# Performance work log

Hardware: AMD Instinct MI355X
Metric: run time of the kernel (lower is better)

## Reference

```python
import jax, jax.numpy as jnp
import numpy as np

B, D, H, E, K = 8192, 1024, 256, 16, 4


def setup_inputs() -> dict:
    key = jax.random.key(0)
    ks = jax.random.split(key, 6)
    s_d = D ** -0.5
    s_h = H ** -0.5
    return {
        "x": jax.random.normal(ks[0], (B, D), dtype=jnp.float32),
        "route_w": jax.random.normal(ks[1], (E, D), dtype=jnp.float32) * s_d,
        "w1": jax.random.normal(ks[2], (E, H, D), dtype=jnp.float32) * s_d,
        "b1": jax.random.normal(ks[3], (E, H), dtype=jnp.float32) * s_d,
        "w2": jax.random.normal(ks[4], (E, D, H), dtype=jnp.float32) * s_h,
        "b2": jax.random.normal(ks[5], (E, D), dtype=jnp.float32) * s_h,
    }


def _moe_forward(x, route_w, w1, b1, w2, b2):
    # Router: logits (B, E) -> top-k softmax weights scattered back to (B, E).
    logits = x @ route_w.T
    top_vals, top_idx = jax.lax.top_k(logits, K)
    top_w = jax.nn.softmax(top_vals, axis=-1)
    rows = jnp.arange(x.shape[0])[:, None]
    weights = jnp.zeros_like(logits).at[rows, top_idx].set(top_w)  # (B, E)

    # Experts: out = sum_e w[:, e] * relu(relu(x W1e^T + b1e) W2e^T + b2e)
    # Non-selected experts have weight 0, so dense-then-weight matches the
    # original masked gather/scatter math exactly (dropout = 0).
    def step(out, params_e):
        W1, bb1, W2, bb2, we = params_e
        h = jax.nn.relu(x @ W1.T + bb1)       # (B, H)
        y = jax.nn.relu(h @ W2.T + bb2)       # (B, D)
        return out + y * we[:, None], None

    out0 = jnp.zeros_like(x)
    out, _ = jax.lax.scan(step, out0, (w1, b1, w2, b2, weights.T))
    return out


def reference(x, route_w, w1, b1, w2, b2):
    return _moe_forward(x, route_w, w1, b1, w2, b2)
```

## Files before the change

### kernel.cpp

```cpp
#include <hip/hip_runtime.h>
#include <stdint.h>

typedef unsigned short u16;
typedef __attribute__((ext_vector_type(8))) short bf16x8;
typedef __attribute__((ext_vector_type(4))) float f32x4;
typedef __attribute__((ext_vector_type(8))) u16 u16x8;
typedef __attribute__((ext_vector_type(4))) u16 u16x4;

#define NTOK 8192
#define DDIM 1024
#define HDIM 256
#define NEXP 16
#define MAXT 272
#define MAXSLOT (MAXT * 128)

__device__ __forceinline__ u16 f2bf(float f) {
  uint32_t u = __builtin_bit_cast(uint32_t, f);
  u += 0x7FFFu + ((u >> 16) & 1u);
  return (u16)(u >> 16);
}
__device__ __forceinline__ float bf2f(u16 h) {
  return __builtin_bit_cast(float, (uint32_t)h << 16);
}

__device__ __forceinline__ void gll16(const void* g, void* l) {
  __builtin_amdgcn_global_load_lds((const __attribute__((address_space(1))) void*)g,
                                   (__attribute__((address_space(3))) void*)l,
                                   16, 0, 0);
}

__global__ __launch_bounds__(256) void cvt_kernel(const float* __restrict__ in,
                                                  u16* __restrict__ out) {
  size_t i = ((size_t)blockIdx.x * 256 + threadIdx.x) * 8;
  const float4 a = *(const float4*)(in + i);
  const float4 b = *(const float4*)(in + i + 4);
  u16x8 o;
  o[0] = f2bf(a.x); o[1] = f2bf(a.y); o[2] = f2bf(a.z); o[3] = f2bf(a.w);
  o[4] = f2bf(b.x); o[5] = f2bf(b.y); o[6] = f2bf(b.z); o[7] = f2bf(b.w);
  *(u16x8*)(out + i) = o;
}

__global__ __launch_bounds__(256) void zero_out_kernel(float* __restrict__ p) {
  size_t i = ((size_t)blockIdx.x * 256 + threadIdx.x) * 4;
  *(float4*)(p + i) = (float4){0.f, 0.f, 0.f, 0.f};
}

__global__ __launch_bounds__(256) void router_kernel(const float* __restrict__ x,
                                                     const float* __restrict__ rw,
                                                     int* __restrict__ epack,
                                                     float* __restrict__ ew,
                                                     u16* __restrict__ xbf) {
  __shared__ __align__(16) uint8_t rwlds[65536];
  const int tid = threadIdx.x;

#pragma unroll
  for (int i = 0; i < 16; ++i) {
    int byte = (i * 256 + tid) * 16;
    int sw = byte ^ (((byte >> 8) & 7) << 4);
    *(float4*)(rwlds + sw) = *(const float4*)((const uint8_t*)rw + byte);
  }
  __syncthreads();

  const int lane = tid & 63, wid = tid >> 6;
  const int s = lane & 15;
  const int tok = blockIdx.x * 16 + wid * 4 + (lane >> 4);
  const float* xrow = x + (size_t)tok * DDIM;
  u16* xbrow = xbf + (size_t)tok * DDIM;

  double acc[NEXP];
#pragma unroll
  for (int e = 0; e < NEXP; ++e) acc[e] = 0.0;

#pragma unroll 4
  for (int g = 0; g < 16; ++g) {
    const int d = s * 64 + g * 4;
    float4 xv = *(const float4*)(xrow + d);
    u16x4 o;
    o[0] = f2bf(xv.x); o[1] = f2bf(xv.y); o[2] = f2bf(xv.z); o[3] = f2bf(xv.w);
    *(u16x4*)(xbrow + d) = o;
    const double x0 = xv.x, x1 = xv.y, x2 = xv.z, x3 = xv.w;
    const int roff = (s * 256 + g * 16) ^ ((s & 7) << 4);
#pragma unroll
    for (int e = 0; e < NEXP; ++e) {
      float4 rv = *(const float4*)(rwlds + e * 4096 + roff);
      acc[e] = fma(x0, (double)rv.x, acc[e]);
      acc[e] = fma(x1, (double)rv.y, acc[e]);
      acc[e] = fma(x2, (double)rv.z, acc[e]);
      acc[e] = fma(x3, (double)rv.w, acc[e]);
    }
  }

#define FOLD(H, M)                                                   \
  _Pragma("unroll") for (int i = 0; i < H; ++i) {                    \
    double send = (lane & M) ? acc[i] : acc[i + H];                  \
    double recv = __shfl_xor(send, M);                               \
    acc[i] = ((lane & M) ? acc[i + H] : acc[i]) + recv;              \
  }
  FOLD(8, 1)
  FOLD(4, 2)
  FOLD(2, 4)
  FOLD(1, 8)
#undef FOLD
  const int e_mine = ((lane & 1) << 3) | ((lane & 2) << 1) |
                     ((lane & 4) >> 1) | ((lane & 8) >> 3);

  double val = acc[0];
  double tv[4]; int tidx[4];
#pragma unroll
  for (int k = 0; k < 4; ++k) {
    double bv = val; int be = e_mine;
#pragma unroll
    for (int m = 1; m < 16; m <<= 1) {
      double ov = __shfl_xor(bv, m);
      int oe = __shfl_xor(be, m);
      if (ov > bv || (ov == bv && oe < be)) { bv = ov; be = oe; }
    }
    tv[k] = bv; tidx[k] = be;
    if (e_mine == be) val = -1.0e300;
  }

  if ((lane & 15) == 0) {
    float m0 = (float)tv[0];
    float w[4]; float sum = 0.f;
#pragma unroll
    for (int k = 0; k < 4; ++k) { w[k] = expf((float)tv[k] - m0); sum += w[k]; }
    epack[tok] = tidx[0] | (tidx[1] << 8) | (tidx[2] << 16) | (tidx[3] << 24);
#pragma unroll
    for (int k = 0; k < 4; ++k) ew[tok * 4 + k] = w[k] / sum;
  }
}

__global__ __launch_bounds__(1024) void compact_kernel(const int* __restrict__ epack,
                                                       const float* __restrict__ ew,
                                                       int* __restrict__ texp,
                                                       int* __restrict__ perm,
                                                       float* __restrict__ wsl,
                                                       int* __restrict__ islot) {
  __shared__ int wave_cnt[16][NEXP];
  __shared__ int counts_sm[NEXP];
  __shared__ int wtot[16], wave_off[16];
  const int e = blockIdx.x;
  const int tid = threadIdx.x, lane = tid & 63, w = tid >> 6;

  int ep[8]; unsigned m[8];
#pragma unroll
  for (int j = 0; j < 8; ++j) {
    ep[j] = epack[tid * 8 + j];
    m[j] = (1u << (ep[j] & 255)) | (1u << ((ep[j] >> 8) & 255)) |
           (1u << ((ep[j] >> 16) & 255)) | (1u << ((ep[j] >> 24) & 255));
  }
#pragma unroll
  for (int ee = 0; ee < NEXP; ++ee) {
    int c = 0;
#pragma unroll
    for (int j = 0; j < 8; ++j) c += (m[j] >> ee) & 1u;
#pragma unroll
    for (int off = 32; off > 0; off >>= 1) c += __shfl_xor(c, off);
    if (lane == 0) wave_cnt[w][ee] = c;
  }
  unsigned fm = 0;
#pragma unroll
  for (int j = 0; j < 8; ++j) fm |= ((m[j] >> e) & 1u) << j;
  int s = __popc(fm);
  int incl = s;
#pragma unroll
  for (int d = 1; d < 64; d <<= 1) {
    int t2 = __shfl_up(incl, d);
    if (lane >= d) incl += t2;
  }
  if (lane == 63) wtot[w] = incl;
  __syncthreads();
  if (tid < NEXP) {
    int c = 0;
    for (int w2 = 0; w2 < 16; ++w2) c += wave_cnt[w2][tid];
    counts_sm[tid] = c;
  }
  if (tid == 0) {
    int run = 0;
    for (int w2 = 0; w2 < 16; ++w2) { wave_off[w2] = run; run += wtot[w2]; }
  }
  __syncthreads();
  int base = 0;
  for (int ee = 0; ee < NEXP; ++ee)
    if (ee < e) base += ((counts_sm[ee] + 127) >> 7) << 7;
  int pos = base + wave_off[w] + (incl - s);
#pragma unroll
  for (int j = 0; j < 8; ++j) {
    if ((fm >> j) & 1u) {
      int tok = tid * 8 + j;
      int b0 = ep[j] & 255, b1 = (ep[j] >> 8) & 255, b2_ = (ep[j] >> 16) & 255;
      int k = (b0 == e) ? 0 : ((b1 == e) ? 1 : ((b2_ == e) ? 2 : 3));
      perm[pos] = tok;
      wsl[pos] = ew[tok * 4 + k];
      islot[tok * 4 + k] = pos;
      ++pos;
    }
  }
  int cnt = counts_sm[e];
  int pad = (((cnt + 127) >> 7) << 7) - cnt;
  if (tid < pad) { perm[base + cnt + tid] = 0; wsl[base + cnt + tid] = 0.f; }
  if (e == 0 && tid == 0) {
    int tc = 0;
    for (int ee = 0; ee < NEXP; ++ee) {
      int nt = (counts_sm[ee] + 127) >> 7;
      for (int i = 0; i < nt; ++i) texp[tc++] = ee;
    }
    for (; tc < MAXT; ++tc) texp[tc] = -1;
  }
}

__device__ __forceinline__ void stage_rows(const u16* __restrict__ base, int ld,
                                           int kbase, uint8_t* dst, int tid) {
#pragma unroll
  for (int i = 0; i < 4; ++i) {
    int u = i * 256 + tid;
    int row = u >> 3, g = u & 7;
    gll16(base + (size_t)row * ld + kbase + ((g ^ (row & 7)) << 3), dst + u * 16);
  }
}
__device__ __forceinline__ void stage_gather(const u16* __restrict__ xbf,
                                             const int tok[4], int kbase,
                                             uint8_t* dst, int tid) {
#pragma unroll
  for (int i = 0; i < 4; ++i) {
    int u = i * 256 + tid;
    int row = u >> 3, g = u & 7;
    gll16(xbf + (size_t)tok[i] * DDIM + kbase + ((g ^ (row & 7)) << 3), dst + u * 16);
  }
}

__device__ __forceinline__ void mma_tile(const uint8_t* Ab, const uint8_t* Bb,
                                         f32x4 acc[4][4], int wm, int wn,
                                         int lrow, int lk) {
#pragma unroll
  for (int s = 0; s < 2; ++s) {
    bf16x8 af[4], bfr[4];
#pragma unroll
    for (int f = 0; f < 4; ++f) {
      int ar = wm * 64 + f * 16 + lrow;
      af[f] = *(const bf16x8*)(Ab + ar * 128 + ((((s << 2) | lk) ^ (ar & 7)) << 4));
      int br = wn * 64 + f * 16 + lrow;
      bfr[f] = *(const bf16x8*)(Bb + br * 128 + ((((s << 2) | lk) ^ (br & 7)) << 4));
    }
#pragma unroll
    for (int i = 0; i < 4; ++i)
#pragma unroll
      for (int j = 0; j < 4; ++j)
        acc[i][j] = __builtin_amdgcn_mfma_f32_16x16x32_bf16(af[i], bfr[j], acc[i][j], 0, 0, 0);
  }
}

__global__ __launch_bounds__(256) void gemm1_kernel(const u16* __restrict__ xbf,
                                                    const u16* __restrict__ w1bf,
                                                    const float* __restrict__ b1,
                                                    const int* __restrict__ texp,
                                                    const int* __restrict__ perm,
                                                    u16* __restrict__ Hc, int t0) {
  __shared__ __align__(16) uint8_t Ab[16384];
  __shared__ __align__(16) uint8_t Bb[16384];
  const int tl = blockIdx.y;
  const int t = t0 + tl;
  const int e = (t < MAXT) ? texp[t] : -1;
  if (e < 0) return;
  const int n0 = blockIdx.x * 128;
  const int tid = threadIdx.x;
  const int lane = tid & 63, wid = tid >> 6;
  const int wm = wid >> 1, wn = wid & 1;
  const int lrow = lane & 15, lk = lane >> 4;

  int tok[4];
#pragma unroll
  for (int i = 0; i < 4; ++i) tok[i] = perm[t * 128 + ((i * 256 + tid) >> 3)];
  const u16* Bsrc = w1bf + ((size_t)e * HDIM + n0) * DDIM;

  f32x4 acc[4][4];
#pragma unroll
  for (int i = 0; i < 4; ++i)
#pragma unroll
    for (int j = 0; j < 4; ++j) acc[i][j] = (f32x4){0.f, 0.f, 0.f, 0.f};

  for (int kt = 0; kt < 16; ++kt) {
    stage_gather(xbf, tok, kt * 64, Ab, tid);
    stage_rows(Bsrc, DDIM, kt * 64, Bb, tid);
    __syncthreads();
    mma_tile(Ab, Bb, acc, wm, wn, lrow, lk);
    __syncthreads();
  }
#pragma unroll
  for (int j = 0; j < 4; ++j) {
    int n = n0 + wn * 64 + j * 16 + lrow;
    float bias = b1[e * HDIM + n];
#pragma unroll
    for (int i = 0; i < 4; ++i) {
      int rloc = tl * 128 + wm * 64 + i * 16 + lk * 4;
#pragma unroll
      for (int r = 0; r < 4; ++r) {
        float h = fmaxf(acc[i][j][r] + bias, 0.f);
        Hc[((size_t)rloc + r) * HDIM + n] = f2bf(h);
      }
    }
  }
}

__global__ __launch_bounds__(256) void gemm2_main_kernel(const u16* __restrict__ Hc,
                                                         const u16* __restrict__ w2bf,
                                                         const float* __restrict__ b2,
                                                         const int* __restrict__ texp,
                                                         u16* __restrict__ ybuf,
                                                         int nbase, int NC) {
  __shared__ __align__(16) uint8_t Ab[16384];
  __shared__ __align__(16) uint8_t Bb[16384];
  const int t = blockIdx.y;
  const int e = texp[t];
  if (e < 0) return;
  const int nl0 = blockIdx.x * 128;
  const int tid = threadIdx.x;
  const int lane = tid & 63, wid = tid >> 6;
  const int wm = wid >> 1, wn = wid & 1;
  const int lrow = lane & 15, lk = lane >> 4;

  const u16* Asrc = Hc + (size_t)t * 128 * HDIM;
  const u16* Bsrc = w2bf + ((size_t)e * DDIM + nbase + nl0) * HDIM;

  f32x4 acc[4][4];
#pragma unroll
  for (int i = 0; i < 4; ++i)
#pragma unroll
    for (int j = 0; j < 4; ++j) acc[i][j] = (f32x4){0.f, 0.f, 0.f, 0.f};

  for (int kt = 0; kt < 4; ++kt) {
    stage_rows(Asrc, HDIM, kt * 64, Ab, tid);
    stage_rows(Bsrc, HDIM, kt * 64, Bb, tid);
    __syncthreads();
    mma_tile(Ab, Bb, acc, wm, wn, lrow, lk);
    __syncthreads();
  }
  float bias[4];
#pragma unroll
  for (int j = 0; j < 4; ++j)
    bias[j] = b2[e * DDIM + nbase + nl0 + wn * 64 + j * 16 + lrow];
#pragma unroll
  for (int i = 0; i < 4; ++i) {
#pragma unroll
    for (int r = 0; r < 4; ++r) {
      int slot = t * 128 + wm * 64 + i * 16 + lk * 4 + r;
#pragma unroll
      for (int j = 0; j < 4; ++j) {
        int nloc = nl0 + wn * 64 + j * 16 + lrow;
        float h = fmaxf(acc[i][j][r] + bias[j], 0.f);
        ybuf[(size_t)slot * NC + nloc] = f2bf(h);
      }
    }
  }
}

__global__ __launch_bounds__(256) void gemm2_fb_kernel(const u16* __restrict__ Hc,
                                                       const u16* __restrict__ w2bf,
                                                       const float* __restrict__ b2,
                                                       const int* __restrict__ texp,
                                                       const int* __restrict__ perm,
                                                       const float* __restrict__ wsl,
                                                       float* __restrict__ out, int t0) {
  __shared__ __align__(16) uint8_t Ab[16384];
  __shared__ __align__(16) uint8_t Bb[16384];
  const int tl = blockIdx.y;
  const int t = t0 + tl;
  const int e = (t < MAXT) ? texp[t] : -1;
  if (e < 0) return;
  const int tid = threadIdx.x;
  const int lane = tid & 63, wid = tid >> 6;
  const int wm = wid >> 1, wn = wid & 1;
  const int lrow = lane & 15, lk = lane >> 4;

  const u16* Asrc = Hc + (size_t)tl * 128 * HDIM;
  const u16* Bsrc = w2bf + ((size_t)e * DDIM + blockIdx.x * 128) * HDIM;

  f32x4 acc[4][4];
#pragma unroll
  for (int i = 0; i < 4; ++i)
#pragma unroll
    for (int j = 0; j < 4; ++j) acc[i][j] = (f32x4){0.f, 0.f, 0.f, 0.f};

  for (int kt = 0; kt < 4; ++kt) {
    stage_rows(Asrc, HDIM, kt * 64, Ab, tid);
    stage_rows(Bsrc, HDIM, kt * 64, Bb, tid);
    __syncthreads();
    mma_tile(Ab, Bb, acc, wm, wn, lrow, lk);
    __syncthreads();
  }
  float bias[4];
#pragma unroll
  for (int j = 0; j < 4; ++j)
    bias[j] = b2[e * DDIM + blockIdx.x * 128 + wn * 64 + j * 16 + lrow];
#pragma unroll
  for (int i = 0; i < 4; ++i) {
#pragma unroll
    for (int r = 0; r < 4; ++r) {
      int slot = t * 128 + wm * 64 + i * 16 + lk * 4 + r;
      int tokn = perm[slot];
      float w = wsl[slot];
#pragma unroll
      for (int j = 0; j < 4; ++j) {
        int n = blockIdx.x * 128 + wn * 64 + j * 16 + lrow;
        float h = fmaxf(acc[i][j][r] + bias[j], 0.f);
        atomicAdd(&out[(size_t)tokn * DDIM + n], w * h);
      }
    }
  }
}

__global__ __launch_bounds__(256) void combine_kernel(const u16* __restrict__ ybuf,
                                                      const float* __restrict__ ew,
                                                      const int* __restrict__ islot,
                                                      float* __restrict__ out,
                                                      int n0, int NC, int cshift) {
  int gid = blockIdx.x * 256 + threadIdx.x;
  int t = gid >> cshift;
  int c = (gid & ((1 << cshift) - 1)) << 2;
  const int4 sl = *(const int4*)(islot + t * 4);
  const float4 w = *(const float4*)(ew + t * 4);
  float4 a = {0.f, 0.f, 0.f, 0.f};
#define ACC(SL, W)                                             \
  {                                                            \
    u16x4 y = *(const u16x4*)(ybuf + (size_t)(SL)*NC + c);     \
    a.x += (W)*bf2f(y[0]); a.y += (W)*bf2f(y[1]);              \
    a.z += (W)*bf2f(y[2]); a.w += (W)*bf2f(y[3]);              \
  }
  ACC(sl.x, w.x); ACC(sl.y, w.y); ACC(sl.z, w.z); ACC(sl.w, w.w);
#undef ACC
  *(float4*)(out + (size_t)t * DDIM + n0 + c) = a;
}

extern "C" void kernel_launch(void* const* d_in, const int* in_sizes, int n_in,
                              void* d_out, int out_size, void* d_ws, size_t ws_size,
                              hipStream_t stream) {
  const float* x = (const float*)d_in[0];
  const float* route_w = (const float*)d_in[1];
  const float* w1 = (const float*)d_in[2];
  const float* b1 = (const float*)d_in[3];
  const float* w2 = (const float*)d_in[4];
  const float* b2 = (const float*)d_in[5];
  float* out = (float*)d_out;

  uint8_t* ws = (uint8_t*)d_ws;
  const size_t OFF_EPACK = 0;
  const size_t OFF_EW    = 32768;
  const size_t OFF_ISLOT = 163840;
  const size_t OFF_TEXP  = 294912;
  const size_t OFF_PERM  = 296960;
  const size_t OFF_WSL   = 436224;
  const size_t OFF_X     = 1048576;
  const size_t OFF_W1    = OFF_X + (size_t)NTOK * DDIM * 2;
  const size_t OFF_W2    = OFF_W1 + (size_t)NEXP * HDIM * DDIM * 2;
  const size_t OFF_HC    = OFF_W2 + (size_t)NEXP * DDIM * HDIM * 2;
  const size_t OFF_Y     = OFF_HC + (size_t)MAXSLOT * HDIM * 2;

  int* epack  = (int*)(ws + OFF_EPACK);
  float* ew   = (float*)(ws + OFF_EW);
  int* islot  = (int*)(ws + OFF_ISLOT);
  int* texp   = (int*)(ws + OFF_TEXP);
  int* perm   = (int*)(ws + OFF_PERM);
  float* wsl  = (float*)(ws + OFF_WSL);
  u16* xbf    = (u16*)(ws + OFF_X);
  u16* w1bf   = (u16*)(ws + OFF_W1);
  u16* w2bf   = (u16*)(ws + OFF_W2);
  u16* Hc     = (u16*)(ws + OFF_HC);
  u16* ybuf   = (u16*)(ws + OFF_Y);

  cvt_kernel<<<dim3((NEXP * HDIM * DDIM) / 2048), 256, 0, stream>>>(w1, w1bf);
  cvt_kernel<<<dim3((NEXP * DDIM * HDIM) / 2048), 256, 0, stream>>>(w2, w2bf);
  router_kernel<<<dim3(NTOK / 16), 256, 0, stream>>>(x, route_w, epack, ew, xbf);
  compact_kernel<<<dim3(NEXP), 1024, 0, stream>>>(epack, ew, texp, perm, wsl, islot);

  int ybN = 0;
  for (int cand = 1024; cand >= 128; cand >>= 1) {
    if (ws_size >= OFF_Y + (size_t)MAXSLOT * cand * 2) { ybN = cand; break; }
  }

  if (ybN > 0) {
    gemm1_kernel<<<dim3(HDIM / 128, MAXT), 256, 0, stream>>>(xbf, w1bf, b1, texp, perm, Hc, 0);
    int cshift = __builtin_ctz(ybN >> 2);
    for (int nb = 0; nb < DDIM; nb += ybN) {
      gemm2_main_kernel<<<dim3(ybN / 128, MAXT), 256, 0, stream>>>(
          Hc, w2bf, b2, texp, ybuf, nb, ybN);
      combine_kernel<<<dim3((NTOK << cshift) / 256), 256, 0, stream>>>(
          ybuf, ew, islot, out, nb, ybN, cshift);
    }
  } else {
    long room = (long)ws_size - (long)OFF_HC;
    int CT = (int)(room / 65536);
    if (CT > MAXT) CT = MAXT;
    if (CT < 16) CT = 16;
    zero_out_kernel<<<dim3((NTOK * DDIM) / 1024), 256, 0, stream>>>(out);
    for (int t0 = 0; t0 < MAXT; t0 += CT) {
      int ct = (MAXT - t0 < CT) ? (MAXT - t0) : CT;
      gemm1_kernel<<<dim3(HDIM / 128, ct), 256, 0, stream>>>(xbf, w1bf, b1, texp, perm, Hc, t0);
      gemm2_fb_kernel<<<dim3(DDIM / 128, ct), 256, 0, stream>>>(
          Hc, w2bf, b2, texp, perm, wsl, out, t0);
    }
  }
}
```

Before: 150.6 us.

## Halve GEMM M-tile to 64 rows and double-buffer LDS staging

Splits each 128-token expert tile into two 64-row M-tiles for gemm1 and both gemm2 kernels, doubling the grid size. This gives more blocks to fill the CUs and fewer accumulators per thread. Also adds double-buffered LDS with a prologue load, so the next K-slice's global-to-LDS copy overlaps the current MFMA work and one barrier per iteration is removed. The cost is less reuse of the B (weight) tile per block, which raises weight traffic, plus more LDS per block (48KB), which may limit occupancy.

Result: faster. 138.5 us (-8.0%).

```diff
diff --git a/kernel.cpp b/kernel.cpp
--- a/kernel.cpp
+++ b/kernel.cpp
@@ -12,6 +12,7 @@
 #define HDIM 256
 #define NEXP 16
 #define MAXT 272
+#define MAXMT (MAXT * 2)
 #define MAXSLOT (MAXT * 128)
 
 __device__ __forceinline__ u16 f2bf(float f) {
@@ -209,8 +210,8 @@
   }
 }
 
-__device__ __forceinline__ void stage_rows(const u16* __restrict__ base, int ld,
-                                           int kbase, uint8_t* dst, int tid) {
+__device__ __forceinline__ void stage128(const u16* __restrict__ base, int ld,
+                                         int kbase, uint8_t* dst, int tid) {
 #pragma unroll
   for (int i = 0; i < 4; ++i) {
     int u = i * 256 + tid;
@@ -218,32 +219,44 @@
     gll16(base + (size_t)row * ld + kbase + ((g ^ (row & 7)) << 3), dst + u * 16);
   }
 }
-__device__ __forceinline__ void stage_gather(const u16* __restrict__ xbf,
-                                             const int tok[4], int kbase,
-                                             uint8_t* dst, int tid) {
-#pragma unroll
-  for (int i = 0; i < 4; ++i) {
+__device__ __forceinline__ void stage64(const u16* __restrict__ base, int ld,
+                                        int kbase, uint8_t* dst, int tid) {
+#pragma unroll
+  for (int i = 0; i < 2; ++i) {
     int u = i * 256 + tid;
     int row = u >> 3, g = u & 7;
-    gll16(xbf + (size_t)tok[i] * DDIM + kbase + ((g ^ (row & 7)) << 3), dst + u * 16);
-  }
-}
-
-__device__ __forceinline__ void mma_tile(const uint8_t* Ab, const uint8_t* Bb,
-                                         f32x4 acc[4][4], int wm, int wn,
-                                         int lrow, int lk) {
+    gll16(base + (size_t)row * ld + kbase + ((g ^ (row & 7)) << 3), dst + u * 16);
+  }
+}
+__device__ __forceinline__ void stage_gather64(const u16* __restrict__ xbf,
+                                               const int tok[2], int kbase,
+                                               uint8_t* dst, int tid) {
+#pragma unroll
+  for (int i = 0; i < 2; ++i) {
+    int u = i * 256 + tid;
+    int g = u & 7;
+    gll16(xbf + (size_t)tok[i] * DDIM + kbase + ((g ^ ((u >> 3) & 7)) << 3), dst + u * 16);
+  }
+}
+
+__device__ __forceinline__ void mma64(const uint8_t* Ab, const uint8_t* Bb,
+                                      f32x4 acc[2][4], int wm, int wn,
+                                      int lrow, int lk) {
 #pragma unroll
   for (int s = 0; s < 2; ++s) {
-    bf16x8 af[4], bfr[4];
+    bf16x8 af[2], bfr[4];
+#pragma unroll
+    for (int f = 0; f < 2; ++f) {
+      int ar = wm * 32 + f * 16 + lrow;
+      af[f] = *(const bf16x8*)(Ab + ar * 128 + ((((s << 2) | lk) ^ (ar & 7)) << 4));
+    }
 #pragma unroll
     for (int f = 0; f < 4; ++f) {
-      int ar = wm * 64 + f * 16 + lrow;
-      af[f] = *(const bf16x8*)(Ab + ar * 128 + ((((s << 2) | lk) ^ (ar & 7)) << 4));
       int br = wn * 64 + f * 16 + lrow;
       bfr[f] = *(const bf16x8*)(Bb + br * 128 + ((((s << 2) | lk) ^ (br & 7)) << 4));
     }
 #pragma unroll
-    for (int i = 0; i < 4; ++i)
+    for (int i = 0; i < 2; ++i)
 #pragma unroll
       for (int j = 0; j < 4; ++j)
         acc[i][j] = __builtin_amdgcn_mfma_f32_16x16x32_bf16(af[i], bfr[j], acc[i][j], 0, 0, 0);
@@ -255,12 +268,10 @@
                                                     const float* __restrict__ b1,
                                                     const int* __restrict__ texp,
                                                     const int* __restrict__ perm,
-                                                    u16* __restrict__ Hc, int t0) {
-  __shared__ __align__(16) uint8_t Ab[16384];
-  __shared__ __align__(16) uint8_t Bb[16384];
-  const int tl = blockIdx.y;
-  const int t = t0 + tl;
-  const int e = (t < MAXT) ? texp[t] : -1;
+                                                    u16* __restrict__ Hc, int mt0) {
+  __shared__ __align__(16) uint8_t smem[2][24576];
+  const int mt = mt0 + blockIdx.y;
+  const int e = (mt < MAXMT) ? texp[mt >> 1] : -1;
   if (e < 0) return;
   const int n0 = blockIdx.x * 128;
   const int tid = threadIdx.x;
@@ -268,31 +279,37 @@
   const int wm = wid >> 1, wn = wid & 1;
   const int lrow = lane & 15, lk = lane >> 4;
 
-  int tok[4];
-#pragma unroll
-  for (int i = 0; i < 4; ++i) tok[i] = perm[t * 128 + ((i * 256 + tid) >> 3)];
+  int tok[2];
+#pragma unroll
+  for (int i = 0; i < 2; ++i) tok[i] = perm[mt * 64 + ((i * 256 + tid) >> 3)];
   const u16* Bsrc = w1bf + ((size_t)e * HDIM + n0) * DDIM;
 
-  f32x4 acc[4][4];
-#pragma unroll
-  for (int i = 0; i < 4; ++i)
+  f32x4 acc[2][4];
+#pragma unroll
+  for (int i = 0; i < 2; ++i)
 #pragma unroll
     for (int j = 0; j < 4; ++j) acc[i][j] = (f32x4){0.f, 0.f, 0.f, 0.f};
 
+  stage_gather64(xbf, tok, 0, smem[0], tid);
+  stage128(Bsrc, DDIM, 0, smem[0] + 8192, tid);
+  __syncthreads();
+  int cur = 0;
   for (int kt = 0; kt < 16; ++kt) {
-    stage_gather(xbf, tok, kt * 64, Ab, tid);
-    stage_rows(Bsrc, DDIM, kt * 64, Bb, tid);
+    if (kt < 15) {
+      stage_gather64(xbf, tok, (kt + 1) * 64, smem[cur ^ 1], tid);
+      stage128(Bsrc, DDIM, (kt + 1) * 64, smem[cur ^ 1] + 8192, tid);
+    }
+    mma64(smem[cur], smem[cur] + 8192, acc, wm, wn, lrow, lk);
     __syncthreads();
-    mma_tile(Ab, Bb, acc, wm, wn, lrow, lk);
-    __syncthreads();
+    cur ^= 1;
   }
 #pragma unroll
   for (int j = 0; j < 4; ++j) {
     int n = n0 + wn * 64 + j * 16 + lrow;
     float bias = b1[e * HDIM + n];
 #pragma unroll
-    for (int i = 0; i < 4; ++i) {
-      int rloc = tl * 128 + wm * 64 + i * 16 + lk * 4;
+    for (int i = 0; i < 2; ++i) {
+      int rloc = (mt - mt0) * 64 + wm * 32 + i * 16 + lk * 4;
 #pragma unroll
       for (int r = 0; r < 4; ++r) {
         float h = fmaxf(acc[i][j][r] + bias, 0.f);
@@ -308,10 +325,9 @@
                                                          const int* __restrict__ texp,
                                                          u16* __restrict__ ybuf,
                                                          int nbase, int NC) {
-  __shared__ __align__(16) uint8_t Ab[16384];
-  __shared__ __align__(16) uint8_t Bb[16384];
-  const int t = blockIdx.y;
-  const int e = texp[t];
+  __shared__ __align__(16) uint8_t smem[2][24576];
+  const int mt = blockIdx.y;
+  const int e = texp[mt >> 1];
   if (e < 0) return;
   const int nl0 = blockIdx.x * 128;
   const int tid = threadIdx.x;
@@ -319,31 +335,37 @@
   const int wm = wid >> 1, wn = wid & 1;
   const int lrow = lane & 15, lk = lane >> 4;
 
-  const u16* Asrc = Hc + (size_t)t * 128 * HDIM;
+  const u16* Asrc = Hc + (size_t)mt * 64 * HDIM;
   const u16* Bsrc = w2bf + ((size_t)e * DDIM + nbase + nl0) * HDIM;
 
-  f32x4 acc[4][4];
-#pragma unroll
-  for (int i = 0; i < 4; ++i)
+  f32x4 acc[2][4];
+#pragma unroll
+  for (int i = 0; i < 2; ++i)
 #pragma unroll
     for (int j = 0; j < 4; ++j) acc[i][j] = (f32x4){0.f, 0.f, 0.f, 0.f};
 
+  stage64(Asrc, HDIM, 0, smem[0], tid);
+  stage128(Bsrc, HDIM, 0, smem[0] + 8192, tid);
+  __syncthreads();
+  int cur = 0;
   for (int kt = 0; kt < 4; ++kt) {
-    stage_rows(Asrc, HDIM, kt * 64, Ab, tid);
-    stage_rows(Bsrc, HDIM, kt * 64, Bb, tid);
+    if (kt < 3) {
+      stage64(Asrc, HDIM, (kt + 1) * 64, smem[cur ^ 1], tid);
+      stage128(Bsrc, HDIM, (kt + 1) * 64, smem[cur ^ 1] + 8192, tid);
+    }
+    mma64(smem[cur], smem[cur] + 8192, acc, wm, wn, lrow, lk);
     __syncthreads();
-    mma_tile(Ab, Bb, acc, wm, wn, lrow, lk);
-    __syncthreads();
+    cur ^= 1;
   }
   float bias[4];
 #pragma unroll
   for (int j = 0; j < 4; ++j)
     bias[j] = b2[e * DDIM + nbase + nl0 + wn * 64 + j * 16 + lrow];
 #pragma unroll
-  for (int i = 0; i < 4; ++i) {
+  for (int i = 0; i < 2; ++i) {
 #pragma unroll
     for (int r = 0; r < 4; ++r) {
-      int slot = t * 128 + wm * 64 + i * 16 + lk * 4 + r;
+      int slot = mt * 64 + wm * 32 + i * 16 + lk * 4 + r;
 #pragma unroll
       for (int j = 0; j < 4; ++j) {
         int nloc = nl0 + wn * 64 + j * 16 + lrow;
@@ -360,48 +382,53 @@
                                                        const int* __restrict__ texp,
                                                        const int* __restrict__ perm,
                                                        const float* __restrict__ wsl,
-                                                       float* __restrict__ out, int t0) {
-  __shared__ __align__(16) uint8_t Ab[16384];
-  __shared__ __align__(16) uint8_t Bb[16384];
-  const int tl = blockIdx.y;
-  const int t = t0 + tl;
-  const int e = (t < MAXT) ? texp[t] : -1;
+                                                       float* __restrict__ out, int mt0) {
+  __shared__ __align__(16) uint8_t smem[2][24576];
+  const int mt = mt0 + blockIdx.y;
+  const int e = (mt < MAXMT) ? texp[mt >> 1] : -1;
   if (e < 0) return;
+  const int nl0 = blockIdx.x * 128;
   const int tid = threadIdx.x;
   const int lane = tid & 63, wid = tid >> 6;
   const int wm = wid >> 1, wn = wid & 1;
   const int lrow = lane & 15, lk = lane >> 4;
 
-  const u16* Asrc = Hc + (size_t)tl * 128 * HDIM;
-  const u16* Bsrc = w2bf + ((size_t)e * DDIM + blockIdx.x * 128) * HDIM;
-
-  f32x4 acc[4][4];
-#pragma unroll
-  for (int i = 0; i < 4; ++i)
+  const u16* Asrc = Hc + (size_t)(mt - mt0) * 64 * HDIM;
+  const u16* Bsrc = w2bf + ((size_t)e * DDIM + nl0) * HDIM;
+
+  f32x4 acc[2][4];
+#pragma unroll
+  for (int i = 0; i < 2; ++i)
 #pragma unroll
     for (int j = 0; j < 4; ++j) acc[i][j] = (f32x4){0.f, 0.f, 0.f, 0.f};
 
+  stage64(Asrc, HDIM, 0, smem[0], tid);
+  stage128(Bsrc, HDIM, 0, smem[0] + 8192, tid);
+  __syncthreads();
+  int cur = 0;
   for (int kt = 0; kt < 4; ++kt) {
-    stage_rows(Asrc, HDIM, kt * 64, Ab, tid);
-    stage_rows(Bsrc, HDIM, kt * 64, Bb, tid);
+    if (kt < 3) {
+      stage64(Asrc, HDIM, (kt + 1) * 64, smem[cur ^ 1], tid);
+      stage128(Bsrc, HDIM, (kt + 1) * 64, smem[cur ^ 1] + 8192, tid);
+    }
+    mma64(smem[cur], smem[cur] + 8192, acc, wm, wn, lrow, lk);
     __syncthreads();
-    mma_tile(Ab, Bb, acc, wm, wn, lrow, lk);
-    __syncthreads();
+    cur ^= 1;
   }
   float bias[4];
 #pragma unroll
   for (int j = 0; j < 4; ++j)
-    bias[j] = b2[e * DDIM + blockIdx.x * 128 + wn * 64 + j * 16 + lrow];
-#pragma unroll
-  for (int i = 0; i < 4; ++i) {
+    bias[j] = b2[e * DDIM + nl0 + wn * 64 + j * 16 + lrow];
+#pragma unroll
+  for (int i = 0; i < 2; ++i) {
 #pragma unroll
     for (int r = 0; r < 4; ++r) {
-      int slot = t * 128 + wm * 64 + i * 16 + lk * 4 + r;
+      int slot = mt * 64 + wm * 32 + i * 16 + lk * 4 + r;
       int tokn = perm[slot];
       float w = wsl[slot];
 #pragma unroll
       for (int j = 0; j < 4; ++j) {
-        int n = blockIdx.x * 128 + wn * 64 + j * 16 + lrow;
+        int n = nl0 + wn * 64 + j * 16 + lrow;
         float h = fmaxf(acc[i][j][r] + bias[j], 0.f);
         atomicAdd(&out[(size_t)tokn * DDIM + n], w * h);
       }
@@ -478,10 +505,10 @@
   }
 
   if (ybN > 0) {
-    gemm1_kernel<<<dim3(HDIM / 128, MAXT), 256, 0, stream>>>(xbf, w1bf, b1, texp, perm, Hc, 0);
+    gemm1_kernel<<<dim3(HDIM / 128, MAXMT), 256, 0, stream>>>(xbf, w1bf, b1, texp, perm, Hc, 0);
     int cshift = __builtin_ctz(ybN >> 2);
     for (int nb = 0; nb < DDIM; nb += ybN) {
-      gemm2_main_kernel<<<dim3(ybN / 128, MAXT), 256, 0, stream>>>(
+      gemm2_main_kernel<<<dim3(ybN / 128, MAXMT), 256, 0, stream>>>(
           Hc, w2bf, b2, texp, ybuf, nb, ybN);
       combine_kernel<<<dim3((NTOK << cshift) / 256), 256, 0, stream>>>(
           ybuf, ew, islot, out, nb, ybN, cshift);
@@ -494,9 +521,10 @@
     zero_out_kernel<<<dim3((NTOK * DDIM) / 1024), 256, 0, stream>>>(out);
     for (int t0 = 0; t0 < MAXT; t0 += CT) {
       int ct = (MAXT - t0 < CT) ? (MAXT - t0) : CT;
-      gemm1_kernel<<<dim3(HDIM / 128, ct), 256, 0, stream>>>(xbf, w1bf, b1, texp, perm, Hc, t0);
-      gemm2_fb_kernel<<<dim3(DDIM / 128, ct), 256, 0, stream>>>(
-          Hc, w2bf, b2, texp, perm, wsl, out, t0);
-    }
-  }
-}
+      gemm1_kernel<<<dim3(HDIM / 128, ct * 2), 256, 0, stream>>>(
+          xbf, w1bf, b1, texp, perm, Hc, t0 * 2);
+      gemm2_fb_kernel<<<dim3(DDIM / 128, ct * 2), 256, 0, stream>>>(
+          Hc, w2bf, b2, texp, perm, wsl, out, t0 * 2);
+    }
+  }
+}
```
